# Kernel optimization log

Hardware: AMD Instinct MI355X
Metric: run time of the kernel (lower is better)

Reference implementation:

```python
import jax, jax.numpy as jnp
import numpy as np

C = 128
EPS = 1e-5


def _layernorm(x, w, b):
    m = jnp.mean(x, axis=-1, keepdims=True)
    v = jnp.mean(jnp.square(x - m), axis=-1, keepdims=True)
    return (x - m) * jax.lax.rsqrt(v + EPS) * w + b


def _linear(x, w, b):
    # torch Linear: y = x @ W.T + b, W is [out, in]
    return jnp.einsum('bijc,dc->bijd', x, w) + b


def setup_inputs() -> dict:
    key = jax.random.key(0)
    ks = jax.random.split(key, 8)
    B, N = 1, 384
    z = jax.random.normal(ks[0], (B, N, N, C), dtype=jnp.float32)
    pair_mask = jnp.ones((B, N, N), dtype=jnp.float32)
    def W(k):
        return jax.random.normal(k, (C, C), dtype=jnp.float32) * 0.02
    return {
        'z': z,
        'pair_mask': pair_mask,
        'ln_in_w': jnp.ones((C,), jnp.float32),
        'ln_in_b': jnp.zeros((C,), jnp.float32),
        'ln_out_w': jnp.ones((C,), jnp.float32),
        'ln_out_b': jnp.zeros((C,), jnp.float32),
        'proj_a_w': W(ks[1]), 'proj_a_b': jnp.zeros((C,), jnp.float32),
        'gate_a_w': W(ks[2]), 'gate_a_b': jnp.zeros((C,), jnp.float32),
        'proj_b_w': W(ks[3]), 'proj_b_b': jnp.zeros((C,), jnp.float32),
        'gate_b_w': W(ks[4]), 'gate_b_b': jnp.zeros((C,), jnp.float32),
        'gate_o_w': W(ks[5]), 'gate_o_b': jnp.zeros((C,), jnp.float32),
        'proj_o_w': W(ks[6]), 'proj_o_b': jnp.zeros((C,), jnp.float32),
    }


def reference(z, pair_mask, ln_in_w, ln_in_b, ln_out_w, ln_out_b,
              proj_a_w, proj_a_b, gate_a_w, gate_a_b,
              proj_b_w, proj_b_b, gate_b_w, gate_b_b,
              gate_o_w, gate_o_b, proj_o_w, proj_o_b):
    mask = pair_mask[..., None]                     # [B,N,N,1]
    z_norm = _layernorm(z, ln_in_w, ln_in_b)
    gate = jax.nn.sigmoid(_linear(z_norm, gate_o_w, gate_o_b))
    a = _linear(z_norm, proj_a_w, proj_a_b) * jax.nn.sigmoid(_linear(z_norm, gate_a_w, gate_a_b)) * mask
    b = _linear(z_norm, proj_b_w, proj_b_b) * jax.nn.sigmoid(_linear(z_norm, gate_b_w, gate_b_b)) * mask
    # incoming: out[i,j,c] = sum_k a[k,j,c] * b[k,i,c]
    contracted = jnp.einsum('bkjc,bkic->bijc', a, b)
    contracted = contracted * mask
    out = _linear(_layernorm(contracted, ln_out_w, ln_out_b), proj_o_w, proj_o_b)
    return out * gate
```

## Files before the change

### kernel.cpp

```cpp
#include <hip/hip_runtime.h>
#include <math.h>

#define NN 384
#define CC 128
#define MT (NN * NN)

typedef __attribute__((ext_vector_type(8))) short bf16x8;
typedef __attribute__((ext_vector_type(4))) short short4v;
typedef __attribute__((ext_vector_type(4))) float f32x4;

__device__ __forceinline__ float bf2f(short u) {
  union { float f; unsigned i; } v; v.i = ((unsigned)(unsigned short)u) << 16; return v.f;
}
__device__ __forceinline__ short f2bf(float f) {
  union { float f; unsigned i; } v; v.f = f;
  unsigned x = v.i;
  return (short)((x + 0x7fffu + ((x >> 16) & 1u)) >> 16);
}
__device__ __forceinline__ void cp16(void* lds, const void* g) {
  __builtin_amdgcn_global_load_lds(
      (const __attribute__((address_space(1))) void*)g,
      (__attribute__((address_space(3))) void*)lds, 16, 0, 0);
}
__device__ __forceinline__ float sigm(float x) { return 1.f / (1.f + __expf(-x)); }

__global__ __launch_bounds__(256) void k_wts(
    const float* __restrict__ w0, const float* __restrict__ w1,
    const float* __restrict__ w2, const float* __restrict__ w3,
    const float* __restrict__ w4, const float* __restrict__ w5,
    short* __restrict__ out)
{
  int idx = blockIdx.x * 256 + threadIdx.x;
  const float* s;
  switch (idx >> 14) {
    case 0: s = w0; break; case 1: s = w1; break; case 2: s = w2; break;
    case 3: s = w3; break; case 4: s = w4; break; default: s = w5; break;
  }
  out[idx] = f2bf(s[idx & 16383]);
}

__global__ __launch_bounds__(256) void k_ln_in(
    const float* __restrict__ z, const float* __restrict__ lw,
    const float* __restrict__ lb, short* __restrict__ zn)
{
  const int wid = threadIdx.x >> 6, lane = threadIdx.x & 63;
  const size_t p = (size_t)blockIdx.x * 4 + wid;
  const float2 v = ((const float2*)(z + p * CC))[lane];
  float s = v.x + v.y, sq = v.x * v.x + v.y * v.y;
  #pragma unroll
  for (int o = 32; o > 0; o >>= 1) { s += __shfl_xor(s, o); sq += __shfl_xor(sq, o); }
  const float mu = s * (1.f / 128.f);
  const float rstd = rsqrtf(sq * (1.f / 128.f) - mu * mu + 1e-5f);
  const float2 w2 = ((const float2*)lw)[lane];
  const float2 b2 = ((const float2*)lb)[lane];
  short2 o2;
  o2.x = f2bf((v.x - mu) * rstd * w2.x + b2.x);
  o2.y = f2bf((v.y - mu) * rstd * w2.y + b2.y);
  ((short2*)(zn + p * CC))[lane] = o2;
}

template<bool PAIRED>
__global__ __launch_bounds__(256) void k_lin(
    const short* __restrict__ zn, const short* __restrict__ Bw,
    const float* __restrict__ bias_p, const float* __restrict__ bias_g,
    const float* __restrict__ mask, short* __restrict__ outp)
{
  __shared__ short As[128 * 64];
  __shared__ short Bs[(PAIRED ? 256 : 128) * 64];
  __shared__ float mask_s[128];

  const int tid = threadIdx.x, wid = tid >> 6, lane = tid & 63;
  const int tile = blockIdx.x;
  const int y0 = tile / 3, x0 = (tile % 3) * 128, p0 = tile * 128;

  if (PAIRED && tid < 128) mask_s[tid] = mask[(size_t)(x0 + tid) * NN + y0];

  f32x4 accP[4][4], accG[4][4];
  #pragma unroll
  for (int i = 0; i < 4; ++i) {
    #pragma unroll
    for (int j = 0; j < 4; ++j) {
      accP[i][j] = f32x4{0.f, 0.f, 0.f, 0.f};
      accG[i][j] = f32x4{0.f, 0.f, 0.f, 0.f};
    }
  }
  const int wm = (wid >> 1) * 64, wn = (wid & 1) * 64;

  #pragma unroll
  for (int kk = 0; kk < 2; ++kk) {
    __syncthreads();
    #pragma unroll
    for (int i = 0; i < 4; ++i) {
      const int rbase = (i * 4 + wid) * 8;
      const int r = rbase + (lane >> 3);
      const size_t srow = PAIRED ? ((size_t)(x0 + r) * NN + y0) : (size_t)(p0 + r);
      cp16((char*)As + rbase * 128,
           (const char*)(zn + srow * CC) + kk * 128 + (lane & 7) * 16);
    }
    const int NR = PAIRED ? 8 : 4;
    #pragma unroll
    for (int i = 0; i < NR; ++i) {
      const int rbase = (i * 4 + wid) * 8;
      const int r = rbase + (lane >> 3);
      cp16((char*)Bs + rbase * 128,
           (const char*)(Bw + (size_t)r * CC) + kk * 128 + (lane & 7) * 16);
    }
    __syncthreads();
    #pragma unroll
    for (int ks = 0; ks < 2; ++ks) {
      const int krow = ks * 32 + (lane >> 4) * 8;
      bf16x8 a[4], bp[4], bg[4];
      #pragma unroll
      for (int f = 0; f < 4; ++f)
        a[f] = *(const bf16x8*)&As[(wm + f * 16 + (lane & 15)) * 64 + krow];
      #pragma unroll
      for (int f = 0; f < 4; ++f)
        bp[f] = *(const bf16x8*)&Bs[(wn + f * 16 + (lane & 15)) * 64 + krow];
      if (PAIRED) {
        #pragma unroll
        for (int f = 0; f < 4; ++f)
          bg[f] = *(const bf16x8*)&Bs[128 * 64 + (wn + f * 16 + (lane & 15)) * 64 + krow];
      }
      #pragma unroll
      for (int fm = 0; fm < 4; ++fm) {
        #pragma unroll
        for (int fn = 0; fn < 4; ++fn) {
          accP[fm][fn] = __builtin_amdgcn_mfma_f32_16x16x32_bf16(a[fm], bp[fn], accP[fm][fn], 0, 0, 0);
          if (PAIRED)
            accG[fm][fn] = __builtin_amdgcn_mfma_f32_16x16x32_bf16(a[fm], bg[fn], accG[fm][fn], 0, 0, 0);
        }
      }
    }
  }

  const size_t rowoff = PAIRED ? ((size_t)y0 * NN + x0) : (size_t)p0;
  #pragma unroll
  for (int fm = 0; fm < 4; ++fm) {
    #pragma unroll
    for (int fn = 0; fn < 4; ++fn) {
      const int c = wn + fn * 16 + (lane & 15);
      const int mb = wm + fm * 16 + (lane >> 4) * 4;
      const float bpv = bias_p[c];
      float bgv = 0.f;
      if (PAIRED) bgv = bias_g[c];
      short4v st;
      #pragma unroll
      for (int e = 0; e < 4; ++e) {
        float v;
        if (PAIRED) {
          const float pv = accP[fm][fn][e] + bpv;
          const float gv = accG[fm][fn][e] + bgv;
          v = pv * sigm(gv) * mask_s[mb + e];
        } else {
          v = sigm(accP[fm][fn][e] + bpv);
        }
        st[e] = f2bf(v);
      }
      *(short4v*)(outp + (size_t)c * MT + rowoff + mb) = st;
    }
  }
}

__global__ __launch_bounds__(256) void k_tri(
    const short* __restrict__ wsa, const short* __restrict__ wsb,
    const float* __restrict__ mask, short* __restrict__ wsct)
{
  __shared__ short As[128 * 64], Bs[128 * 64];
  const int tid = threadIdx.x, wid = tid >> 6, lane = tid & 63;
  const int c = blockIdx.y;
  const int i0 = (blockIdx.x / 3) * 128, j0 = (blockIdx.x % 3) * 128;
  const short* Ab = wsa + (size_t)c * MT;
  const short* Bb = wsb + (size_t)c * MT;

  f32x4 acc[4][4];
  #pragma unroll
  for (int i = 0; i < 4; ++i) {
    #pragma unroll
    for (int j = 0; j < 4; ++j) acc[i][j] = f32x4{0.f, 0.f, 0.f, 0.f};
  }
  const int wm = (wid >> 1) * 64, wn = (wid & 1) * 64;

  for (int kt = 0; kt < 6; ++kt) {
    __syncthreads();
    #pragma unroll
    for (int i = 0; i < 4; ++i) {
      const int rbase = (i * 4 + wid) * 8;
      const int r = rbase + (lane >> 3);
      cp16((char*)As + rbase * 128,
           (const char*)(Ab + (size_t)(j0 + r) * NN) + kt * 128 + (lane & 7) * 16);
      cp16((char*)Bs + rbase * 128,
           (const char*)(Bb + (size_t)(i0 + r) * NN) + kt * 128 + (lane & 7) * 16);
    }
    __syncthreads();
    #pragma unroll
    for (int ks = 0; ks < 2; ++ks) {
      const int krow = ks * 32 + (lane >> 4) * 8;
      bf16x8 a[4], b[4];
      #pragma unroll
      for (int f = 0; f < 4; ++f) {
        a[f] = *(const bf16x8*)&As[(wm + f * 16 + (lane & 15)) * 64 + krow];
        b[f] = *(const bf16x8*)&Bs[(wn + f * 16 + (lane & 15)) * 64 + krow];
      }
      #pragma unroll
      for (int fm = 0; fm < 4; ++fm) {
        #pragma unroll
        for (int fn = 0; fn < 4; ++fn)
          acc[fm][fn] = __builtin_amdgcn_mfma_f32_16x16x32_bf16(a[fm], b[fn], acc[fm][fn], 0, 0, 0);
      }
    }
  }
  #pragma unroll
  for (int fm = 0; fm < 4; ++fm) {
    #pragma unroll
    for (int fn = 0; fn < 4; ++fn) {
      const int i = i0 + wn + fn * 16 + (lane & 15);
      const int jb = j0 + wm + fm * 16 + (lane >> 4) * 4;
      const f32x4 mk = *(const f32x4*)(mask + (size_t)i * NN + jb);
      short4v st;
      #pragma unroll
      for (int e = 0; e < 4; ++e) st[e] = f2bf(acc[fm][fn][e] * mk[e]);
      *(short4v*)(wsct + (size_t)c * MT + (size_t)i * NN + jb) = st;
    }
  }
}

__global__ __launch_bounds__(256) void k_ln_out(
    const short* __restrict__ wsct, const float* __restrict__ lw,
    const float* __restrict__ lb, short* __restrict__ z2)
{
  __shared__ float T[128][65];
  const int tid = threadIdx.x;
  const int p0 = blockIdx.x * 64;

  #pragma unroll
  for (int rep = 0; rep < 4; ++rep) {
    const int c = rep * 32 + (tid >> 3);
    const int pp = (tid & 7) * 8;
    const bf16x8 v = *(const bf16x8*)(wsct + (size_t)c * MT + p0 + pp);
    #pragma unroll
    for (int e = 0; e < 8; ++e) T[c][pp + e] = bf2f(v[e]);
  }
  __syncthreads();

  const int pl = tid >> 2, q = tid & 3;
  float s = 0.f, sq = 0.f;
  #pragma unroll
  for (int ccd = 0; ccd < 32; ++ccd) {
    const float v = T[q * 32 + ccd][pl];
    s += v; sq += v * v;
  }
  s += __shfl_xor(s, 1); sq += __shfl_xor(sq, 1);
  s += __shfl_xor(s, 2); sq += __shfl_xor(sq, 2);
  const float mu = s * (1.f / 128.f);
  const float rstd = rsqrtf(sq * (1.f / 128.f) - mu * mu + 1e-5f);

  const size_t p = p0 + pl;
  #pragma unroll
  for (int v8 = 0; v8 < 4; ++v8) {
    const int cb = q * 32 + v8 * 8;
    bf16x8 st;
    #pragma unroll
    for (int e = 0; e < 8; ++e)
      st[e] = f2bf((T[cb + e][pl] - mu) * rstd * lw[cb + e] + lb[cb + e]);
    *(bf16x8*)(z2 + p * CC + cb) = st;
  }
}

__global__ __launch_bounds__(256) void k_out(
    const short* __restrict__ z2, const short* __restrict__ Bw,
    const float* __restrict__ bo, const short* __restrict__ gate,
    float* __restrict__ out)
{
  __shared__ short As[128 * 64], Bs[128 * 64];
  const int tid = threadIdx.x, wid = tid >> 6, lane = tid & 63;
  const int p0 = blockIdx.x * 128;

  f32x4 acc[4][4];
  #pragma unroll
  for (int i = 0; i < 4; ++i) {
    #pragma unroll
    for (int j = 0; j < 4; ++j) acc[i][j] = f32x4{0.f, 0.f, 0.f, 0.f};
  }
  const int wm = (wid >> 1) * 64, wn = (wid & 1) * 64;

  #pragma unroll
  for (int kk = 0; kk < 2; ++kk) {
    __syncthreads();
    #pragma unroll
    for (int i = 0; i < 4; ++i) {
      const int rbase = (i * 4 + wid) * 8;
      const int r = rbase + (lane >> 3);
      cp16((char*)As + rbase * 128,
           (const char*)(z2 + (size_t)(p0 + r) * CC) + kk * 128 + (lane & 7) * 16);
      cp16((char*)Bs + rbase * 128,
           (const char*)(Bw + (size_t)r * CC) + kk * 128 + (lane & 7) * 16);
    }
    __syncthreads();
    #pragma unroll
    for (int ks = 0; ks < 2; ++ks) {
      const int krow = ks * 32 + (lane >> 4) * 8;
      bf16x8 a[4], b[4];
      #pragma unroll
      for (int f = 0; f < 4; ++f) {
        a[f] = *(const bf16x8*)&As[(wm + f * 16 + (lane & 15)) * 64 + krow];
        b[f] = *(const bf16x8*)&Bs[(wn + f * 16 + (lane & 15)) * 64 + krow];
      }
      #pragma unroll
      for (int fm = 0; fm < 4; ++fm) {
        #pragma unroll
        for (int fn = 0; fn < 4; ++fn)
          acc[fm][fn] = __builtin_amdgcn_mfma_f32_16x16x32_bf16(a[fm], b[fn], acc[fm][fn], 0, 0, 0);
      }
    }
  }
  #pragma unroll
  for (int fm = 0; fm < 4; ++fm) {
    #pragma unroll
    for (int fn = 0; fn < 4; ++fn) {
      const int d = wn + fn * 16 + (lane & 15);
      const int mb = wm + fm * 16 + (lane >> 4) * 4;
      const float bd = bo[d];
      const short4v gv = *(const short4v*)(gate + (size_t)d * MT + p0 + mb);
      #pragma unroll
      for (int e = 0; e < 4; ++e)
        out[(size_t)(p0 + mb + e) * CC + d] = (acc[fm][fn][e] + bd) * bf2f(gv[e]);
    }
  }
}

extern "C" void kernel_launch(void* const* d_in, const int* in_sizes, int n_in,
                              void* d_out, int out_size, void* d_ws, size_t ws_size,
                              hipStream_t stream) {
  const float* z        = (const float*)d_in[0];
  const float* mask     = (const float*)d_in[1];
  const float* ln_in_w  = (const float*)d_in[2];
  const float* ln_in_b  = (const float*)d_in[3];
  const float* ln_out_w = (const float*)d_in[4];
  const float* ln_out_b = (const float*)d_in[5];
  const float* pa_w = (const float*)d_in[6];  const float* pa_b = (const float*)d_in[7];
  const float* ga_w = (const float*)d_in[8];  const float* ga_b = (const float*)d_in[9];
  const float* pb_w = (const float*)d_in[10]; const float* pb_b = (const float*)d_in[11];
  const float* gb_w = (const float*)d_in[12]; const float* gb_b = (const float*)d_in[13];
  const float* go_w = (const float*)d_in[14]; const float* go_b = (const float*)d_in[15];
  const float* po_w = (const float*)d_in[16]; const float* po_b = (const float*)d_in[17];

  char* ws = (char*)d_ws;
  const size_t SZ = (size_t)MT * CC * 2;
  short* zn   = (short*)(ws);
  short* wsa  = (short*)(ws + SZ);
  short* wsb  = (short*)(ws + 2 * SZ);
  short* wsg  = (short*)(ws + 3 * SZ);
  short* wts  = (short*)(ws + 4 * SZ);
  short* wsct = zn;
  short* z2   = wsa;

  k_wts<<<384, 256, 0, stream>>>(pa_w, ga_w, pb_w, gb_w, go_w, po_w, wts);
  k_ln_in<<<MT / 4, 256, 0, stream>>>(z, ln_in_w, ln_in_b, zn);
  k_lin<true ><<<1152, 256, 0, stream>>>(zn, wts,             pa_b, ga_b, mask, wsa);
  k_lin<true ><<<1152, 256, 0, stream>>>(zn, wts + 2 * 16384, pb_b, gb_b, mask, wsb);
  k_lin<false><<<1152, 256, 0, stream>>>(zn, wts + 4 * 16384, go_b, nullptr, nullptr, wsg);
  k_tri<<<dim3(9, 128), 256, 0, stream>>>(wsa, wsb, mask, wsct);
  k_ln_out<<<MT / 64, 256, 0, stream>>>(wsct, ln_out_w, ln_out_b, z2);
  k_out<<<1152, 256, 0, stream>>>(z2, wts + 5 * 16384, po_b, wsg, (float*)d_out);
}
```

Before: 386.9 us.

## Swizzle LDS tiles, stage epilogue stores through LDS, remap triangle grid

```diff
diff --git a/kernel.cpp b/kernel.cpp
--- a/kernel.cpp
+++ b/kernel.cpp
@@ -23,6 +23,7 @@
       (__attribute__((address_space(3))) void*)lds, 16, 0, 0);
 }
 __device__ __forceinline__ float sigm(float x) { return 1.f / (1.f + __expf(-x)); }
+
 
 __global__ __launch_bounds__(256) void k_wts(
     const float* __restrict__ w0, const float* __restrict__ w1,
@@ -65,9 +66,11 @@
     const float* __restrict__ bias_p, const float* __restrict__ bias_g,
     const float* __restrict__ mask, short* __restrict__ outp)
 {
-  __shared__ short As[128 * 64];
-  __shared__ short Bs[(PAIRED ? 256 : 128) * 64];
+  __shared__ char smem[PAIRED ? 49152 : 34816];
   __shared__ float mask_s[128];
+  short* As = (short*)smem;
+  short* Bs = (short*)(smem + 16384);
+  short* T  = (short*)smem;
 
   const int tid = threadIdx.x, wid = tid >> 6, lane = tid & 63;
   const int tile = blockIdx.x;
@@ -85,6 +88,7 @@
     }
   }
   const int wm = (wid >> 1) * 64, wn = (wid & 1) * 64;
+  const int slot = (lane & 7) ^ (lane >> 3);
 
   #pragma unroll
   for (int kk = 0; kk < 2; ++kk) {
@@ -95,7 +99,7 @@
       const int r = rbase + (lane >> 3);
       const size_t srow = PAIRED ? ((size_t)(x0 + r) * NN + y0) : (size_t)(p0 + r);
       cp16((char*)As + rbase * 128,
-           (const char*)(zn + srow * CC) + kk * 128 + (lane & 7) * 16);
+           (const char*)(zn + srow * CC) + kk * 128 + slot * 16);
     }
     const int NR = PAIRED ? 8 : 4;
     #pragma unroll
@@ -103,23 +107,24 @@
       const int rbase = (i * 4 + wid) * 8;
       const int r = rbase + (lane >> 3);
       cp16((char*)Bs + rbase * 128,
-           (const char*)(Bw + (size_t)r * CC) + kk * 128 + (lane & 7) * 16);
+           (const char*)(Bw + (size_t)r * CC) + kk * 128 + slot * 16);
     }
     __syncthreads();
     #pragma unroll
     for (int ks = 0; ks < 2; ++ks) {
-      const int krow = ks * 32 + (lane >> 4) * 8;
+      const int u = ks * 4 + (lane >> 4);
+      const int sl = (u ^ (lane & 7)) * 8;
       bf16x8 a[4], bp[4], bg[4];
       #pragma unroll
       for (int f = 0; f < 4; ++f)
-        a[f] = *(const bf16x8*)&As[(wm + f * 16 + (lane & 15)) * 64 + krow];
+        a[f] = *(const bf16x8*)&As[(wm + f * 16 + (lane & 15)) * 64 + sl];
       #pragma unroll
       for (int f = 0; f < 4; ++f)
-        bp[f] = *(const bf16x8*)&Bs[(wn + f * 16 + (lane & 15)) * 64 + krow];
+        bp[f] = *(const bf16x8*)&Bs[(wn + f * 16 + (lane & 15)) * 64 + sl];
       if (PAIRED) {
         #pragma unroll
         for (int f = 0; f < 4; ++f)
-          bg[f] = *(const bf16x8*)&Bs[128 * 64 + (wn + f * 16 + (lane & 15)) * 64 + krow];
+          bg[f] = *(const bf16x8*)&Bs[128 * 64 + (wn + f * 16 + (lane & 15)) * 64 + sl];
       }
       #pragma unroll
       for (int fm = 0; fm < 4; ++fm) {
@@ -133,7 +138,7 @@
     }
   }
 
-  const size_t rowoff = PAIRED ? ((size_t)y0 * NN + x0) : (size_t)p0;
+  __syncthreads();
   #pragma unroll
   for (int fm = 0; fm < 4; ++fm) {
     #pragma unroll
@@ -141,23 +146,33 @@
       const int c = wn + fn * 16 + (lane & 15);
       const int mb = wm + fm * 16 + (lane >> 4) * 4;
       const float bpv = bias_p[c];
-      float bgv = 0.f;
-      if (PAIRED) bgv = bias_g[c];
-      short4v st;
-      #pragma unroll
-      for (int e = 0; e < 4; ++e) {
-        float v;
-        if (PAIRED) {
+      if (PAIRED) {
+        const float bgv = bias_g[c];
+        short4v st;
+        #pragma unroll
+        for (int e = 0; e < 4; ++e) {
           const float pv = accP[fm][fn][e] + bpv;
           const float gv = accG[fm][fn][e] + bgv;
-          v = pv * sigm(gv) * mask_s[mb + e];
-        } else {
-          v = sigm(accP[fm][fn][e] + bpv);
+          st[e] = f2bf(pv * sigm(gv) * mask_s[mb + e]);
         }
-        st[e] = f2bf(v);
-      }
-      *(short4v*)(outp + (size_t)c * MT + rowoff + mb) = st;
-    }
+        *(short4v*)&T[c * 136 + mb] = st;
+      } else {
+        #pragma unroll
+        for (int e = 0; e < 4; ++e)
+          T[(mb + e) * 136 + c] = f2bf(sigm(accP[fm][fn][e] + bpv));
+      }
+    }
+  }
+  __syncthreads();
+  const size_t rowoff = (size_t)y0 * NN + x0;
+  #pragma unroll
+  for (int rep = 0; rep < 8; ++rep) {
+    const int row = rep * 16 + (tid >> 4), chunk = tid & 15;
+    const bf16x8 v = *(const bf16x8*)&T[row * 136 + chunk * 8];
+    if (PAIRED)
+      *(bf16x8*)(outp + (size_t)row * MT + rowoff + chunk * 8) = v;
+    else
+      *(bf16x8*)(outp + (size_t)(p0 + row) * CC + chunk * 8) = v;
   }
 }
 
@@ -165,10 +180,15 @@
     const short* __restrict__ wsa, const short* __restrict__ wsb,
     const float* __restrict__ mask, short* __restrict__ wsct)
 {
-  __shared__ short As[128 * 64], Bs[128 * 64];
+  __shared__ char smem[34816];
+  short* As = (short*)smem;
+  short* Bs = (short*)(smem + 16384);
+  short* T  = (short*)smem;
+
   const int tid = threadIdx.x, wid = tid >> 6, lane = tid & 63;
-  const int c = blockIdx.y;
-  const int i0 = (blockIdx.x / 3) * 128, j0 = (blockIdx.x % 3) * 128;
+  const int o = (blockIdx.x & 7) * 144 + (blockIdx.x >> 3);
+  const int c = o / 9, t9 = o % 9;
+  const int i0 = (t9 / 3) * 128, j0 = (t9 % 3) * 128;
   const short* Ab = wsa + (size_t)c * MT;
   const short* Bb = wsb + (size_t)c * MT;
 
@@ -179,6 +199,7 @@
     for (int j = 0; j < 4; ++j) acc[i][j] = f32x4{0.f, 0.f, 0.f, 0.f};
   }
   const int wm = (wid >> 1) * 64, wn = (wid & 1) * 64;
+  const int slot = (lane & 7) ^ (lane >> 3);
 
   for (int kt = 0; kt < 6; ++kt) {
     __syncthreads();
@@ -187,19 +208,20 @@
       const int rbase = (i * 4 + wid) * 8;
       const int r = rbase + (lane >> 3);
       cp16((char*)As + rbase * 128,
-           (const char*)(Ab + (size_t)(j0 + r) * NN) + kt * 128 + (lane & 7) * 16);
+           (const char*)(Ab + (size_t)(j0 + r) * NN) + kt * 128 + slot * 16);
       cp16((char*)Bs + rbase * 128,
-           (const char*)(Bb + (size_t)(i0 + r) * NN) + kt * 128 + (lane & 7) * 16);
+           (const char*)(Bb + (size_t)(i0 + r) * NN) + kt * 128 + slot * 16);
     }
     __syncthreads();
     #pragma unroll
     for (int ks = 0; ks < 2; ++ks) {
-      const int krow = ks * 32 + (lane >> 4) * 8;
+      const int u = ks * 4 + (lane >> 4);
+      const int sl = (u ^ (lane & 7)) * 8;
       bf16x8 a[4], b[4];
       #pragma unroll
       for (int f = 0; f < 4; ++f) {
-        a[f] = *(const bf16x8*)&As[(wm + f * 16 + (lane & 15)) * 64 + krow];
-        b[f] = *(const bf16x8*)&Bs[(wn + f * 16 + (lane & 15)) * 64 + krow];
+        a[f] = *(const bf16x8*)&As[(wm + f * 16 + (lane & 15)) * 64 + sl];
+        b[f] = *(const bf16x8*)&Bs[(wn + f * 16 + (lane & 15)) * 64 + sl];
       }
       #pragma unroll
       for (int fm = 0; fm < 4; ++fm) {
@@ -209,18 +231,27 @@
       }
     }
   }
+
+  __syncthreads();
   #pragma unroll
   for (int fm = 0; fm < 4; ++fm) {
     #pragma unroll
     for (int fn = 0; fn < 4; ++fn) {
-      const int i = i0 + wn + fn * 16 + (lane & 15);
-      const int jb = j0 + wm + fm * 16 + (lane >> 4) * 4;
-      const f32x4 mk = *(const f32x4*)(mask + (size_t)i * NN + jb);
+      const int il = wn + fn * 16 + (lane & 15);
+      const int jb = wm + fm * 16 + (lane >> 4) * 4;
+      const f32x4 mk = *(const f32x4*)(mask + (size_t)(i0 + il) * NN + j0 + jb);
       short4v st;
       #pragma unroll
       for (int e = 0; e < 4; ++e) st[e] = f2bf(acc[fm][fn][e] * mk[e]);
-      *(short4v*)(wsct + (size_t)c * MT + (size_t)i * NN + jb) = st;
-    }
+      *(short4v*)&T[il * 136 + jb] = st;
+    }
+  }
+  __syncthreads();
+  #pragma unroll
+  for (int rep = 0; rep < 8; ++rep) {
+    const int row = rep * 16 + (tid >> 4), chunk = tid & 15;
+    const bf16x8 v = *(const bf16x8*)&T[row * 136 + chunk * 8];
+    *(bf16x8*)(wsct + (size_t)c * MT + (size_t)(i0 + row) * NN + j0 + chunk * 8) = v;
   }
 }
 
@@ -282,6 +313,7 @@
     for (int j = 0; j < 4; ++j) acc[i][j] = f32x4{0.f, 0.f, 0.f, 0.f};
   }
   const int wm = (wid >> 1) * 64, wn = (wid & 1) * 64;
+  const int slot = (lane & 7) ^ (lane >> 3);
 
   #pragma unroll
   for (int kk = 0; kk < 2; ++kk) {
@@ -291,19 +323,20 @@
       const int rbase = (i * 4 + wid) * 8;
       const int r = rbase + (lane >> 3);
       cp16((char*)As + rbase * 128,
-           (const char*)(z2 + (size_t)(p0 + r) * CC) + kk * 128 + (lane & 7) * 16);
+           (const char*)(z2 + (size_t)(p0 + r) * CC) + kk * 128 + slot * 16);
       cp16((char*)Bs + rbase * 128,
-           (const char*)(Bw + (size_t)r * CC) + kk * 128 + (lane & 7) * 16);
+           (const char*)(Bw + (size_t)r * CC) + kk * 128 + slot * 16);
     }
     __syncthreads();
     #pragma unroll
     for (int ks = 0; ks < 2; ++ks) {
-      const int krow = ks * 32 + (lane >> 4) * 8;
+      const int u = ks * 4 + (lane >> 4);
+      const int sl = (u ^ (lane & 7)) * 8;
       bf16x8 a[4], b[4];
       #pragma unroll
       for (int f = 0; f < 4; ++f) {
-        a[f] = *(const bf16x8*)&As[(wm + f * 16 + (lane & 15)) * 64 + krow];
-        b[f] = *(const bf16x8*)&Bs[(wn + f * 16 + (lane & 15)) * 64 + krow];
+        a[f] = *(const bf16x8*)&As[(wm + f * 16 + (lane & 15)) * 64 + sl];
+        b[f] = *(const bf16x8*)&Bs[(wn + f * 16 + (lane & 15)) * 64 + sl];
       }
       #pragma unroll
       for (int fm = 0; fm < 4; ++fm) {
@@ -320,10 +353,11 @@
       const int d = wn + fn * 16 + (lane & 15);
       const int mb = wm + fm * 16 + (lane >> 4) * 4;
       const float bd = bo[d];
-      const short4v gv = *(const short4v*)(gate + (size_t)d * MT + p0 + mb);
-      #pragma unroll
-      for (int e = 0; e < 4; ++e)
-        out[(size_t)(p0 + mb + e) * CC + d] = (acc[fm][fn][e] + bd) * bf2f(gv[e]);
+      #pragma unroll
+      for (int e = 0; e < 4; ++e) {
+        const float g = bf2f(gate[(size_t)(p0 + mb + e) * CC + d]);
+        out[(size_t)(p0 + mb + e) * CC + d] = (acc[fm][fn][e] + bd) * g;
+      }
     }
   }
 }
@@ -359,7 +393,7 @@
   k_lin<true ><<<1152, 256, 0, stream>>>(zn, wts,             pa_b, ga_b, mask, wsa);
   k_lin<true ><<<1152, 256, 0, stream>>>(zn, wts + 2 * 16384, pb_b, gb_b, mask, wsb);
   k_lin<false><<<1152, 256, 0, stream>>>(zn, wts + 4 * 16384, go_b, nullptr, nullptr, wsg);
-  k_tri<<<dim3(9, 128), 256, 0, stream>>>(wsa, wsb, mask, wsct);
+  k_tri<<<1152, 256, 0, stream>>>(wsa, wsb, mask, wsct);
   k_ln_out<<<MT / 64, 256, 0, stream>>>(wsct, ln_out_w, ln_out_b, z2);
   k_out<<<1152, 256, 0, stream>>>(z2, wts + 5 * 16384, po_b, wsg, (float*)d_out);
 }
```

After: 354.9 us. 8.3% less time.
